# Optimization experiments

Hardware: AMD Instinct MI355X
Metric: run time of the kernel (lower is better)

The kernel has to match this reference:

```python
import jax, jax.numpy as jnp
from jax import lax
import numpy as np

IMG = 1024                      # image_size (square)
RPN_TRAIN_THRES = 0.5
RATIOS = jnp.array([0.5, 1.0, 2.0], jnp.float32)
SCALES = jnp.array([0.2, 0.4, 0.7], jnp.float32)
K_GT = 16


def _conv(x, w, b, stride):
    # NHWC x HWIO -> NHWC, VALID padding (keras Conv2D default)
    return lax.conv_general_dilated(x, w, (stride, stride), 'VALID',
                                    dimension_numbers=('NHWC', 'HWIO', 'NHWC')) + b


def _anchor_set():
    # [-w/2, -h/2, w/2, h/2] for 9 ratio/scale combos
    rs = jnp.sqrt(RATIOS)[:, None]                      # (3,1)
    ws = (SCALES[None, :] * rs).reshape(-1)             # (9,)
    hs = (SCALES[None, :] / rs).reshape(-1)
    return jnp.stack([ws, hs, ws, hs], axis=1) * 0.5 * jnp.array([-1.0, -1.0, 1.0, 1.0], jnp.float32)


def _anchors_pre(h, w):
    # mirrors generate_anchors_pre (incl. tf.transpose reversing axes -> (W,H,4));
    # feature map is square here so the layout matches the original.
    x = jnp.arange(0.0, 1.0, 1.0 / w, dtype=jnp.float32)
    y = jnp.arange(0.0, 1.0, 1.0 / h, dtype=jnp.float32)
    xx, yy = jnp.meshgrid(x, y)                         # (H,W)
    centers = jnp.stack([xx, yy, xx, yy], 0).transpose(2, 1, 0)  # (W,H,4)
    return centers[:, :, None, :] + _anchor_set()       # (W,H,9,4)


def _iou(b1, b2, gw, gh):
    gwh = jnp.array([gw, gh], jnp.float32)
    s1 = jnp.prod(b1[..., 2:] - b1[..., :2] + gwh, axis=-1)
    s2 = jnp.prod(b2[..., 2:] - b2[..., :2] + gwh, axis=-1)
    xa = jnp.maximum(b1[..., 0], b2[..., 0])
    ya = jnp.maximum(b1[..., 1], b2[..., 1])
    xb = jnp.minimum(b1[..., 2], b2[..., 2])
    yb = jnp.minimum(b1[..., 3], b2[..., 3])
    inter = jnp.maximum(xb - xa + gw, 0.0) * jnp.maximum(yb - ya + gh, 0.0)
    return inter / (s1 + s2 - inter)


def setup_inputs() -> dict:
    key = jax.random.key(0)
    ks = jax.random.split(key, 10)
    image = jax.random.uniform(ks[0], (1, IMG, IMG, 3), jnp.float32)
    cxy = jax.random.uniform(ks[1], (K_GT, 2), jnp.float32, 0.2, 0.8)
    wh = jax.random.uniform(ks[2], (K_GT, 2), jnp.float32, 0.1, 0.4)
    gt_boxes = jnp.concatenate([cxy - wh / 2, cxy + wh / 2], axis=1)  # (K,4) x1,y1,x2,y2
    Wb = jax.random.normal(ks[3], (4, 4, 3, 128), jnp.float32) * 0.05
    bb = jnp.zeros((128,), jnp.float32)
    Wi = jax.random.normal(ks[4], (3, 3, 128, 256), jnp.float32) * 0.05
    bi = jnp.zeros((256,), jnp.float32)
    Wc = jax.random.normal(ks[5], (1, 1, 256, 9), jnp.float32) * 0.05
    bc = jnp.zeros((9,), jnp.float32)
    Wr = jax.random.normal(ks[6], (1, 1, 256, 36), jnp.float32) * 0.05
    br = jnp.zeros((36,), jnp.float32)
    return {'image': image, 'gt_boxes': gt_boxes, 'Wb': Wb, 'bb': bb,
            'Wi': Wi, 'bi': bi, 'Wc': Wc, 'bc': bc, 'Wr': Wr, 'br': br}


def reference(image, gt_boxes, Wb, bb, Wi, bi, Wc, bc, Wr, br):
    feats = _conv(image, Wb, bb, 4)            # backbone: (1,256,256,128)
    fmap = _conv(feats, Wi, bi, 1)             # inter_conv: (1,254,254,256)
    fh, fw = fmap.shape[1], fmap.shape[2]
    gw = 1.0 / IMG
    gh = 1.0 / IMG
    anchors = _anchors_pre(fh, fw).reshape(-1, 4)          # (N,4), N = fh*fw*9
    inside = ((anchors[:, 0] >= 0.0) & (anchors[:, 1] >= 0.0) &
              (anchors[:, 2] < 1.0) & (anchors[:, 3] < 1.0))
    iou = _iou(anchors[:, None, :], gt_boxes[None, :, :], gw, gh)  # (N,K)
    max_iou = jnp.max(iou, axis=1)
    iou_in = jnp.where(inside[:, None], iou, -1.0)
    gt_max_iou = jnp.max(iou_in, axis=0)                   # (K,)
    is_gt_best = jnp.any((iou_in == gt_max_iou[None, :]) & inside[:, None], axis=1)
    pos = inside & (is_gt_best | (max_iou >= RPN_TRAIN_THRES))
    labels = jnp.where(inside, 0.0, -1.0)
    labels = jnp.where(pos, 1.0, labels)                   # (N,) in {-1,0,1}
    # RPN classification loss (BCE with logits) over labels != -1
    cls = _conv(fmap, Wc, bc, 1).reshape(-1)               # (N,)
    sel = (labels != -1.0).astype(jnp.float32)
    lbl = jnp.maximum(labels, 0.0)
    bce = lbl * jax.nn.softplus(-cls) + (1.0 - lbl) * jax.nn.softplus(cls)
    cls_loss = jnp.sum(bce * sel) / jnp.sum(sel)
    # smooth-L1 box loss, faithful to the original (it masks bbox_pred, not the diff)
    reg = _conv(fmap, Wr, br, 1).reshape(-1, 4)            # (N,4)
    m = pos.astype(jnp.float32)[:, None]                   # (N,1) bbox_mask
    ab = jnp.abs(reg * m)
    ss = (ab < 1.0).astype(jnp.float32)
    box_loss = ab * ab * 0.5 * ss + (ab - 0.5) * (1.0 - ss)
    bbox_loss = jnp.sum(box_loss) / jnp.sum(m)
    return cls_loss + bbox_loss
```

## Files before the change

kernel.cpp:

```cpp
#include <hip/hip_runtime.h>

#define F2      254
#define NPIX    (F2 * F2)
#define NANCH   (NPIX * 9)
#define KGT     16
#define GWC     (1.0f / 1024.0f)

typedef __attribute__((ext_vector_type(8))) short bf16x8;
typedef __attribute__((ext_vector_type(4))) float f32x4;

struct LossMap {
    int w0[9], h0[9], hsp[9], blk0[10];
};

__device__ unsigned short g_feats[256 * 256 * 128];
__device__ unsigned short g_cls[NPIX * 9];
__device__ unsigned short g_reg[NPIX * 36];
__device__ unsigned short g_W2s[36 * 3 * 64 * 8];
__device__ unsigned short g_Wbs[2 * 8 * 64 * 8];
__device__ float          g_b2[48];
__device__ float          g_acc[4];
__device__ unsigned       g_keys[KGT];
__device__ unsigned       g_done;

__device__ __forceinline__ float b2f(unsigned short h) {
    return __uint_as_float(((unsigned)h) << 16);
}
__device__ __forceinline__ unsigned short f2b(float f) {
    unsigned u = __float_as_uint(f);
    unsigned r = (u + 0x7FFFu + ((u >> 16) & 1u)) >> 16;
    return (unsigned short)r;
}

__device__ __forceinline__ void iou16(float x1, float y1, float x2, float y2,
                                      const float* __restrict__ gt, float* __restrict__ v) {
    float s1 = (x2 - x1 + GWC) * (y2 - y1 + GWC);
#pragma unroll
    for (int k = 0; k < KGT; ++k) {
        float gx1 = gt[k * 4 + 0], gy1 = gt[k * 4 + 1];
        float gx2 = gt[k * 4 + 2], gy2 = gt[k * 4 + 3];
        float s2 = (gx2 - gx1 + GWC) * (gy2 - gy1 + GWC);
        float xa = fmaxf(x1, gx1), ya = fmaxf(y1, gy1);
        float xb = fminf(x2, gx2), yb = fminf(y2, gy2);
        float iw = fmaxf(xb - xa + GWC, 0.0f);
        float ih = fmaxf(yb - ya + GWC, 0.0f);
        float inter = iw * ih;
        v[k] = inter / (s1 + s2 - inter);
    }
}

__device__ __forceinline__ void type_extent(int a, float* hw, float* hh) {
    int ri = a / 3, si = a - ri * 3;
    float rat = (ri == 0) ? 0.5f : (ri == 1) ? 1.0f : 2.0f;
    float scl = (si == 0) ? 0.2f : (si == 1) ? 0.4f : 0.7f;
    float rs = sqrtf(rat);
    *hw = scl * rs * 0.5f;
    *hh = scl / rs * 0.5f;
}

__global__ __launch_bounds__(256) void k_w2(const float* __restrict__ Wi,
                                            const float* __restrict__ bi,
                                            const float* __restrict__ Wc,
                                            const float* __restrict__ bc,
                                            const float* __restrict__ Wr,
                                            const float* __restrict__ br,
                                            const float* __restrict__ Wb,
                                            unsigned* out) {
    int t = threadIdx.x;
    int b = blockIdx.x;
    if (b >= 288) {
        int e = (b - 288) * 256 + t;
        int kt = e >> 9, nt = (e >> 6) & 7, l = e & 63;
        unsigned short w8[8];
#pragma unroll
        for (int j = 0; j < 8; ++j) {
            int k = kt * 32 + ((l >> 4) * 8) + j;
            int oc = nt * 16 + (l & 15);
            w8[j] = (k < 48) ? f2b(Wb[(size_t)k * 128 + oc]) : (unsigned short)0;
        }
        *(ulonglong2*)(g_Wbs + (size_t)e * 8) = *(ulonglong2*)w8;
        return;
    }
    __shared__ float wcr[256][48];
    if (b == 0) {
        if (t < 4) g_acc[t] = 0.0f;
        if (t >= 4 && t < 4 + KGT) g_keys[t - 4] = 0x407FFFFFu;
        if (t == 32) out[0] = 0x3F803F80u;
        if (t == 33) g_done = 0u;
    }
    for (int i = t; i < 2304; i += 256) wcr[i / 9][i % 9] = Wc[i];
    for (int i = t; i < 9216; i += 256) wcr[i / 36][9 + i % 36] = Wr[i];
    for (int i = t; i < 768; i += 256) wcr[i / 3][45 + i % 3] = 0.0f;
    __syncthreads();

    int wave = __builtin_amdgcn_readfirstlane(t >> 6);
    int lane = t & 63;
    int k = b * 4 + wave;
    int o = min(lane, 47);
    const float* wik = Wi + (size_t)k * 256;
    float acc = 0.0f;
#pragma unroll 8
    for (int oc = 0; oc < 256; ++oc)
        acc = fmaf(wik[oc], wcr[oc][o], acc);

    if (lane < 48) {
        int kt = k >> 5, r5 = k & 31, j = r5 & 7, lhi = r5 >> 3;
        int nt = o >> 4, llo = o & 15, l = lhi * 16 + llo;
        g_W2s[(size_t)((kt * 3 + nt) * 64 + l) * 8 + j] = f2b(acc);
    }
    if (b == 0 && t < 48) {
        float a2 = (t < 9) ? bc[t] : ((t < 45) ? br[t - 9] : 0.0f);
        for (int oc = 0; oc < 256; ++oc) a2 = fmaf(bi[oc], wcr[oc][t], a2);
        g_b2[t] = a2;
    }
}

__device__ __forceinline__ bf16x8 ld_a8(const float* ib, int kbase) {
    int r0 = kbase / 12, q0 = kbase - r0 * 12;
    unsigned short a8[8];
    float4 f0 = *(const float4*)(ib + (size_t)r0 * 3072 + q0);
    int k4 = kbase + 4;
    int r1 = k4 / 12, q1 = k4 - r1 * 12;
    float4 f1 = *(const float4*)(ib + (size_t)r1 * 3072 + q1);
    a8[0] = f2b(f0.x); a8[1] = f2b(f0.y); a8[2] = f2b(f0.z); a8[3] = f2b(f0.w);
    a8[4] = f2b(f1.x); a8[5] = f2b(f1.y); a8[6] = f2b(f1.z); a8[7] = f2b(f1.w);
    return *(bf16x8*)a8;
}

__global__ __launch_bounds__(256) void k_conv1gt(const float* __restrict__ img,
                                                 const float* __restrict__ bb,
                                                 const float* __restrict__ gt) {
    __shared__ float red[4][KGT];
    int t = threadIdx.x;
    if (blockIdx.x < 1024) {
        int l = t & 63;
        int quad = l >> 4;
        int tile = blockIdx.x * 4 + (t >> 6);
        int m0 = tile * 16;
        int p = m0 + (l & 15);
        int oy = p >> 8, ox = p & 255;
        const float* ib = img + ((size_t)oy * 4 * 1024 + (size_t)ox * 4) * 3;

        bf16x8 a0 = ld_a8(ib, quad * 8);
        bf16x8 a1 = (quad < 2) ? ld_a8(ib, 32 + quad * 8) : (bf16x8){0, 0, 0, 0, 0, 0, 0, 0};

        f32x4 acc[8];
#pragma unroll
        for (int nt = 0; nt < 8; ++nt) acc[nt] = (f32x4){0.0f, 0.0f, 0.0f, 0.0f};
#pragma unroll
        for (int nt = 0; nt < 8; ++nt) {
            bf16x8 b0 = *(const bf16x8*)(g_Wbs + (size_t)(nt * 64 + l) * 8);
            bf16x8 b1 = *(const bf16x8*)(g_Wbs + (size_t)((8 + nt) * 64 + l) * 8);
            acc[nt] = __builtin_amdgcn_mfma_f32_16x16x32_bf16(a0, b0, acc[nt], 0, 0, 0);
            acc[nt] = __builtin_amdgcn_mfma_f32_16x16x32_bf16(a1, b1, acc[nt], 0, 0, 0);
        }

        int n0 = l & 15;
        int mB = m0 + quad * 4;
#pragma unroll
        for (int nt = 0; nt < 8; ++nt) {
            int oc = nt * 16 + n0;
            float bias = bb[oc];
#pragma unroll
            for (int r = 0; r < 4; ++r) {
                g_feats[(size_t)(mB + r) * 128 + oc] = f2b(acc[nt][r] + bias);
            }
        }
    } else {
        int bid = blockIdx.x - 1024;
        int a = bid >> 5;
        int blk = bid & 31;
        float hw, hh;
        type_extent(a, &hw, &hh);
        float m16[KGT];
#pragma unroll
        for (int k = 0; k < KGT; ++k) m16[k] = -1.0f;
        for (int pix = blk * 256 + t; pix < NPIX; pix += 32 * 256) {
            int w = pix / F2, h = pix - w * F2;
            float cx = (float)w * (1.0f / 254.0f);
            float cy = (float)h * (1.0f / 254.0f);
            float x1 = cx - hw, y1 = cy - hh, x2 = cx + hw, y2 = cy + hh;
            bool inside = (x1 >= 0.0f) && (y1 >= 0.0f) && (x2 < 1.0f) && (y2 < 1.0f);
            if (__ballot(inside) == 0ull) continue;
            if (inside) {
                float v[KGT];
                iou16(x1, y1, x2, y2, gt, v);
#pragma unroll
                for (int k = 0; k < KGT; ++k) m16[k] = fmaxf(m16[k], v[k]);
            }
        }
#pragma unroll
        for (int k = 0; k < KGT; ++k) {
#pragma unroll
            for (int m = 32; m; m >>= 1) m16[k] = fmaxf(m16[k], __shfl_xor(m16[k], m, 64));
        }
        int lane = t & 63, wv = t >> 6;
        if (lane == 0) {
#pragma unroll
            for (int k = 0; k < KGT; ++k) red[wv][k] = m16[k];
        }
        __syncthreads();
        if (t < KGT) {
            float mx = fmaxf(fmaxf(red[0][t], red[1][t]), fmaxf(red[2][t], red[3][t]));
            unsigned u = __float_as_uint(mx);
            unsigned key = (u & 0x80000000u) ? ~u : (u | 0x80000000u);
            atomicMax(&g_keys[t], key);
        }
    }
}

__global__ __launch_bounds__(256) void k_convC() {
    __shared__ unsigned short Bs[12 * 1536];
    int t = threadIdx.x;
    int l = t & 63;
    int quad = l >> 4;
    int tile = blockIdx.x * 4 + (t >> 6);
    int m0 = tile * 32;
    int mA0 = min(m0 + (l & 15), NPIX - 1);
    int mA1 = min(m0 + 16 + (l & 15), NPIX - 1);
    int py0 = mA0 / F2, px0 = mA0 - py0 * F2;
    int py1 = mA1 / F2, px1 = mA1 - py1 * F2;

    f32x4 acc[2][3];
#pragma unroll
    for (int h = 0; h < 2; ++h)
#pragma unroll
        for (int nt = 0; nt < 3; ++nt) acc[h][nt] = (f32x4){0.0f, 0.0f, 0.0f, 0.0f};

    for (int c = 0; c < 3; ++c) {
        __syncthreads();
        {
            const uint4* src = (const uint4*)(g_W2s + (size_t)c * 18432);
            uint4* dst = (uint4*)Bs;
#pragma unroll
            for (int j = 0; j < 9; ++j) dst[t + 256 * j] = src[t + 256 * j];
        }
        __syncthreads();
#pragma unroll
        for (int i = 0; i < 12; ++i) {
            int kt = c * 12 + i;
            int pos = kt >> 2, kc = kt & 3;
            int ky = pos / 3, kx = pos - ky * 3;
            const unsigned short* ap0 =
                g_feats + ((size_t)(py0 + ky) * 256 + (px0 + kx)) * 128 + quad * 8 + kc * 32;
            const unsigned short* ap1 =
                g_feats + ((size_t)(py1 + ky) * 256 + (px1 + kx)) * 128 + quad * 8 + kc * 32;
            bf16x8 a0 = *(const bf16x8*)ap0;
            bf16x8 a1 = *(const bf16x8*)ap1;
            const unsigned short* bp = Bs + (size_t)i * 1536 + l * 8;
            bf16x8 b0 = *(const bf16x8*)(bp);
            bf16x8 b1 = *(const bf16x8*)(bp + 512);
            bf16x8 b2v = *(const bf16x8*)(bp + 1024);
            acc[0][0] = __builtin_amdgcn_mfma_f32_16x16x32_bf16(a0, b0, acc[0][0], 0, 0, 0);
            acc[0][1] = __builtin_amdgcn_mfma_f32_16x16x32_bf16(a0, b1, acc[0][1], 0, 0, 0);
            acc[0][2] = __builtin_amdgcn_mfma_f32_16x16x32_bf16(a0, b2v, acc[0][2], 0, 0, 0);
            acc[1][0] = __builtin_amdgcn_mfma_f32_16x16x32_bf16(a1, b0, acc[1][0], 0, 0, 0);
            acc[1][1] = __builtin_amdgcn_mfma_f32_16x16x32_bf16(a1, b1, acc[1][1], 0, 0, 0);
            acc[1][2] = __builtin_amdgcn_mfma_f32_16x16x32_bf16(a1, b2v, acc[1][2], 0, 0, 0);
        }
    }

    int n0 = l & 15;
#pragma unroll
    for (int h = 0; h < 2; ++h) {
        int mB = m0 + h * 16 + quad * 4;
#pragma unroll
        for (int nt = 0; nt < 3; ++nt) {
            int n = nt * 16 + n0;
            if (n >= 45) continue;
            float bias = g_b2[n];
#pragma unroll
            for (int r = 0; r < 4; ++r) {
                int m = mB + r;
                if (m < NPIX) {
                    float vv = acc[h][nt][r] + bias;
                    if (n < 9) g_cls[(size_t)m * 9 + n] = f2b(vv);
                    else       g_reg[(size_t)m * 36 + (n - 9)] = f2b(vv);
                }
            }
        }
    }
}

__global__ __launch_bounds__(256) void k_loss(const float* __restrict__ gt, unsigned* out,
                                              LossMap lm, int nblocks) {
    __shared__ float red[4][4];
    int t = threadIdx.x;
    int a = 0;
    while (a < 8 && (int)blockIdx.x >= lm.blk0[a + 1]) ++a;
    int idx = ((int)blockIdx.x - lm.blk0[a]) * 256 + t;
    int hsp = lm.hsp[a];
    int w = lm.w0[a] + idx / hsp;
    int h = lm.h0[a] + idx % hsp;
    float sb = 0.0f, ss = 0.0f, sx = 0.0f, sp = 0.0f;
    float hw, hh;
    type_extent(a, &hw, &hh);
    bool inside = false;
    float x1, y1, x2, y2;
    if (w < F2 && h < F2) {
        float cx = (float)w * (1.0f / 254.0f);
        float cy = (float)h * (1.0f / 254.0f);
        x1 = cx - hw; y1 = cy - hh; x2 = cx + hw; y2 = cy + hh;
        inside = (x1 >= 0.0f) && (y1 >= 0.0f) && (x2 < 1.0f) && (y2 < 1.0f);
    }
    if (__ballot(inside) != 0ull) {
        if (inside) {
            int pix = w * F2 + h;
            int n = pix * 9 + a;
            float v[KGT];
            iou16(x1, y1, x2, y2, gt, v);
            float maxi = -1.0f;
            bool best = false;
#pragma unroll
            for (int k = 0; k < KGT; ++k) {
                maxi = fmaxf(maxi, v[k]);
                unsigned e = g_keys[k];
                float gm = __uint_as_float((e & 0x80000000u) ? (e & 0x7FFFFFFFu) : ~e);
                best = best || (v[k] == gm);
            }
            bool ispos = best || (maxi >= 0.5f);
            float c = b2f(g_cls[n]);
            float z = ispos ? -c : c;
            sb = fmaxf(z, 0.0f) + log1pf(expf(-fabsf(z)));
            ss = 1.0f;
            if (ispos) {
                ushort4 rh = *(const ushort4*)(g_reg + (size_t)n * 4);
                float aa;
                aa = fabsf(b2f(rh.x)); sx += (aa < 1.0f) ? 0.5f * aa * aa : aa - 0.5f;
                aa = fabsf(b2f(rh.y)); sx += (aa < 1.0f) ? 0.5f * aa * aa : aa - 0.5f;
                aa = fabsf(b2f(rh.z)); sx += (aa < 1.0f) ? 0.5f * aa * aa : aa - 0.5f;
                aa = fabsf(b2f(rh.w)); sx += (aa < 1.0f) ? 0.5f * aa * aa : aa - 0.5f;
                sp = 1.0f;
            }
        }
    }
#pragma unroll
    for (int m = 32; m; m >>= 1) {
        sb += __shfl_xor(sb, m, 64);
        ss += __shfl_xor(ss, m, 64);
        sx += __shfl_xor(sx, m, 64);
        sp += __shfl_xor(sp, m, 64);
    }
    int lane = t & 63, wv = t >> 6;
    if (lane == 0) { red[wv][0] = sb; red[wv][1] = ss; red[wv][2] = sx; red[wv][3] = sp; }
    __syncthreads();
    if (t < 4) {
        float s = red[0][t] + red[1][t] + red[2][t] + red[3][t];
        atomicAdd(&g_acc[t], s);
    }
    __syncthreads();
    if (t == 0) {
        unsigned prev = atomicAdd(&g_done, 1u);
        if (prev == (unsigned)(nblocks - 1)) {
            float a0 = atomicAdd(&g_acc[0], 0.0f);
            float a1 = atomicAdd(&g_acc[1], 0.0f);
            float a2 = atomicAdd(&g_acc[2], 0.0f);
            float a3 = atomicAdd(&g_acc[3], 0.0f);
            float res = a0 / a1 + a2 / a3;
            unsigned lo = (unsigned)f2b(res);
            unsigned hi = __float_as_uint(res) >> 16;
            out[0] = (hi << 16) | lo;
        }
    }
}

extern "C" void kernel_launch(void* const* d_in, const int* in_sizes, int n_in,
                              void* d_out, int out_size, void* d_ws, size_t ws_size,
                              hipStream_t stream) {
    (void)in_sizes; (void)n_in; (void)out_size; (void)d_ws; (void)ws_size;
    const float* image = (const float*)d_in[0];
    const float* gt    = (const float*)d_in[1];
    const float* Wb    = (const float*)d_in[2];
    const float* bb    = (const float*)d_in[3];
    const float* Wi    = (const float*)d_in[4];
    const float* bi    = (const float*)d_in[5];
    const float* Wc    = (const float*)d_in[6];
    const float* bc    = (const float*)d_in[7];
    const float* Wr    = (const float*)d_in[8];
    const float* br    = (const float*)d_in[9];

    LossMap lm;
    int nb = 0;
    const float RAT[3] = {0.5f, 1.0f, 2.0f};
    const float SCL[3] = {0.2f, 0.4f, 0.7f};
    for (int a = 0; a < 9; ++a) {
        int ri = a / 3, si = a - ri * 3;
        float rs = sqrtf(RAT[ri]);
        float hw = SCL[si] * rs * 0.5f;
        float hh = SCL[si] / rs * 0.5f;
        int wa0 = (int)floorf(254.0f * hw) - 1; if (wa0 < 0) wa0 = 0;
        int wa1 = (int)ceilf(254.0f * (1.0f - hw)) + 1; if (wa1 > 253) wa1 = 253;
        int ha0 = (int)floorf(254.0f * hh) - 1; if (ha0 < 0) ha0 = 0;
        int ha1 = (int)ceilf(254.0f * (1.0f - hh)) + 1; if (ha1 > 253) ha1 = 253;
        int wspan = wa1 - wa0 + 1, hspan = ha1 - ha0 + 1;
        lm.w0[a] = wa0; lm.h0[a] = ha0; lm.hsp[a] = hspan;
        lm.blk0[a] = nb;
        nb += (wspan * hspan + 255) / 256;
    }
    lm.blk0[9] = nb;

    k_w2     <<<292, 256, 0, stream>>>(Wi, bi, Wc, bc, Wr, br, Wb, (unsigned*)d_out);
    k_conv1gt<<<1312, 256, 0, stream>>>(image, bb, gt);
    k_convC  <<<505, 256, 0, stream>>>();
    k_loss   <<<nb, 256, 0, stream>>>(gt, (unsigned*)d_out, lm, nb);
}
```

Baseline: 153.6 us.

## Fuse RPN head conv with loss and move GT-max pass into prep kernel

Fuses the classification/regression conv kernel with the loss kernel. Head outputs are staged in shared memory instead of being written to global g_cls/g_reg and read back. The per-GT max-IoU pass moves from the conv1 kernel into the weight-prep kernel, and conv1 block indices are remapped across XCDs. State reset now happens at the end of the last block rather than in a prep kernel, which cuts one launch and removes a global round trip. The cost is that the loss loop now scans all anchors per tile instead of only the bounded inside region, and it relies on static initialisers for the first call.

```diff
diff --git a/kernel.cpp b/kernel.cpp
--- a/kernel.cpp
+++ b/kernel.cpp
@@ -2,26 +2,23 @@
 
 #define F2      254
 #define NPIX    (F2 * F2)
-#define NANCH   (NPIX * 9)
 #define KGT     16
 #define GWC     (1.0f / 1024.0f)
 
 typedef __attribute__((ext_vector_type(8))) short bf16x8;
 typedef __attribute__((ext_vector_type(4))) float f32x4;
 
-struct LossMap {
-    int w0[9], h0[9], hsp[9], blk0[10];
-};
-
 __device__ unsigned short g_feats[256 * 256 * 128];
-__device__ unsigned short g_cls[NPIX * 9];
-__device__ unsigned short g_reg[NPIX * 36];
 __device__ unsigned short g_W2s[36 * 3 * 64 * 8];
 __device__ unsigned short g_Wbs[2 * 8 * 64 * 8];
 __device__ float          g_b2[48];
-__device__ float          g_acc[4];
-__device__ unsigned       g_keys[KGT];
-__device__ unsigned       g_done;
+__device__ float          g_acc[4] = {0.0f, 0.0f, 0.0f, 0.0f};
+__device__ unsigned       g_keys[KGT] = {
+    0x407FFFFFu, 0x407FFFFFu, 0x407FFFFFu, 0x407FFFFFu,
+    0x407FFFFFu, 0x407FFFFFu, 0x407FFFFFu, 0x407FFFFFu,
+    0x407FFFFFu, 0x407FFFFFu, 0x407FFFFFu, 0x407FFFFFu,
+    0x407FFFFFu, 0x407FFFFFu, 0x407FFFFFu, 0x407FFFFFu};
+__device__ unsigned       g_done = 0u;
 
 __device__ __forceinline__ float b2f(unsigned short h) {
     return __uint_as_float(((unsigned)h) << 16);
@@ -58,116 +55,21 @@
     *hh = scl / rs * 0.5f;
 }
 
-__global__ __launch_bounds__(256) void k_w2(const float* __restrict__ Wi,
-                                            const float* __restrict__ bi,
-                                            const float* __restrict__ Wc,
-                                            const float* __restrict__ bc,
-                                            const float* __restrict__ Wr,
-                                            const float* __restrict__ br,
-                                            const float* __restrict__ Wb,
-                                            unsigned* out) {
+__global__ __launch_bounds__(256) void k_prep(const float* __restrict__ Wi,
+                                              const float* __restrict__ bi,
+                                              const float* __restrict__ Wc,
+                                              const float* __restrict__ bc,
+                                              const float* __restrict__ Wr,
+                                              const float* __restrict__ br,
+                                              const float* __restrict__ Wb,
+                                              const float* __restrict__ gt) {
+    __shared__ float wcr[256][48];
+    __shared__ float red[4][KGT];
     int t = threadIdx.x;
     int b = blockIdx.x;
-    if (b >= 288) {
-        int e = (b - 288) * 256 + t;
-        int kt = e >> 9, nt = (e >> 6) & 7, l = e & 63;
-        unsigned short w8[8];
-#pragma unroll
-        for (int j = 0; j < 8; ++j) {
-            int k = kt * 32 + ((l >> 4) * 8) + j;
-            int oc = nt * 16 + (l & 15);
-            w8[j] = (k < 48) ? f2b(Wb[(size_t)k * 128 + oc]) : (unsigned short)0;
-        }
-        *(ulonglong2*)(g_Wbs + (size_t)e * 8) = *(ulonglong2*)w8;
-        return;
-    }
-    __shared__ float wcr[256][48];
-    if (b == 0) {
-        if (t < 4) g_acc[t] = 0.0f;
-        if (t >= 4 && t < 4 + KGT) g_keys[t - 4] = 0x407FFFFFu;
-        if (t == 32) out[0] = 0x3F803F80u;
-        if (t == 33) g_done = 0u;
-    }
-    for (int i = t; i < 2304; i += 256) wcr[i / 9][i % 9] = Wc[i];
-    for (int i = t; i < 9216; i += 256) wcr[i / 36][9 + i % 36] = Wr[i];
-    for (int i = t; i < 768; i += 256) wcr[i / 3][45 + i % 3] = 0.0f;
-    __syncthreads();
-
-    int wave = __builtin_amdgcn_readfirstlane(t >> 6);
-    int lane = t & 63;
-    int k = b * 4 + wave;
-    int o = min(lane, 47);
-    const float* wik = Wi + (size_t)k * 256;
-    float acc = 0.0f;
-#pragma unroll 8
-    for (int oc = 0; oc < 256; ++oc)
-        acc = fmaf(wik[oc], wcr[oc][o], acc);
-
-    if (lane < 48) {
-        int kt = k >> 5, r5 = k & 31, j = r5 & 7, lhi = r5 >> 3;
-        int nt = o >> 4, llo = o & 15, l = lhi * 16 + llo;
-        g_W2s[(size_t)((kt * 3 + nt) * 64 + l) * 8 + j] = f2b(acc);
-    }
-    if (b == 0 && t < 48) {
-        float a2 = (t < 9) ? bc[t] : ((t < 45) ? br[t - 9] : 0.0f);
-        for (int oc = 0; oc < 256; ++oc) a2 = fmaf(bi[oc], wcr[oc][t], a2);
-        g_b2[t] = a2;
-    }
-}
-
-__device__ __forceinline__ bf16x8 ld_a8(const float* ib, int kbase) {
-    int r0 = kbase / 12, q0 = kbase - r0 * 12;
-    unsigned short a8[8];
-    float4 f0 = *(const float4*)(ib + (size_t)r0 * 3072 + q0);
-    int k4 = kbase + 4;
-    int r1 = k4 / 12, q1 = k4 - r1 * 12;
-    float4 f1 = *(const float4*)(ib + (size_t)r1 * 3072 + q1);
-    a8[0] = f2b(f0.x); a8[1] = f2b(f0.y); a8[2] = f2b(f0.z); a8[3] = f2b(f0.w);
-    a8[4] = f2b(f1.x); a8[5] = f2b(f1.y); a8[6] = f2b(f1.z); a8[7] = f2b(f1.w);
-    return *(bf16x8*)a8;
-}
-
-__global__ __launch_bounds__(256) void k_conv1gt(const float* __restrict__ img,
-                                                 const float* __restrict__ bb,
-                                                 const float* __restrict__ gt) {
-    __shared__ float red[4][KGT];
-    int t = threadIdx.x;
-    if (blockIdx.x < 1024) {
-        int l = t & 63;
-        int quad = l >> 4;
-        int tile = blockIdx.x * 4 + (t >> 6);
-        int m0 = tile * 16;
-        int p = m0 + (l & 15);
-        int oy = p >> 8, ox = p & 255;
-        const float* ib = img + ((size_t)oy * 4 * 1024 + (size_t)ox * 4) * 3;
-
-        bf16x8 a0 = ld_a8(ib, quad * 8);
-        bf16x8 a1 = (quad < 2) ? ld_a8(ib, 32 + quad * 8) : (bf16x8){0, 0, 0, 0, 0, 0, 0, 0};
-
-        f32x4 acc[8];
-#pragma unroll
-        for (int nt = 0; nt < 8; ++nt) acc[nt] = (f32x4){0.0f, 0.0f, 0.0f, 0.0f};
-#pragma unroll
-        for (int nt = 0; nt < 8; ++nt) {
-            bf16x8 b0 = *(const bf16x8*)(g_Wbs + (size_t)(nt * 64 + l) * 8);
-            bf16x8 b1 = *(const bf16x8*)(g_Wbs + (size_t)((8 + nt) * 64 + l) * 8);
-            acc[nt] = __builtin_amdgcn_mfma_f32_16x16x32_bf16(a0, b0, acc[nt], 0, 0, 0);
-            acc[nt] = __builtin_amdgcn_mfma_f32_16x16x32_bf16(a1, b1, acc[nt], 0, 0, 0);
-        }
-
-        int n0 = l & 15;
-        int mB = m0 + quad * 4;
-#pragma unroll
-        for (int nt = 0; nt < 8; ++nt) {
-            int oc = nt * 16 + n0;
-            float bias = bb[oc];
-#pragma unroll
-            for (int r = 0; r < 4; ++r) {
-                g_feats[(size_t)(mB + r) * 128 + oc] = f2b(acc[nt][r] + bias);
-            }
-        }
-    } else {
-        int bid = blockIdx.x - 1024;
+
+    if (b >= 292) {
+        int bid = b - 292;
         int a = bid >> 5;
         int blk = bid & 31;
         float hw, hh;
@@ -206,15 +108,114 @@
             unsigned key = (u & 0x80000000u) ? ~u : (u | 0x80000000u);
             atomicMax(&g_keys[t], key);
         }
-    }
-}
-
-__global__ __launch_bounds__(256) void k_convC() {
-    __shared__ unsigned short Bs[12 * 1536];
+        return;
+    }
+
+    if (b >= 288) {
+        int e = (b - 288) * 256 + t;
+        int kt = e >> 9, nt = (e >> 6) & 7, l = e & 63;
+        unsigned short w8[8];
+#pragma unroll
+        for (int j = 0; j < 8; ++j) {
+            int k = kt * 32 + ((l >> 4) * 8) + j;
+            int oc = nt * 16 + (l & 15);
+            w8[j] = (k < 48) ? f2b(Wb[(size_t)k * 128 + oc]) : (unsigned short)0;
+        }
+        *(ulonglong2*)(g_Wbs + (size_t)e * 8) = *(ulonglong2*)w8;
+        return;
+    }
+
+    for (int i = t; i < 2304; i += 256) wcr[i / 9][i % 9] = Wc[i];
+    for (int i = t; i < 9216; i += 256) wcr[i / 36][9 + i % 36] = Wr[i];
+    for (int i = t; i < 768; i += 256) wcr[i / 3][45 + i % 3] = 0.0f;
+    __syncthreads();
+
+    int wave = __builtin_amdgcn_readfirstlane(t >> 6);
+    int lane = t & 63;
+    int k = b * 4 + wave;
+    int o = min(lane, 47);
+    const float* wik = Wi + (size_t)k * 256;
+    float acc = 0.0f;
+#pragma unroll 8
+    for (int oc = 0; oc < 256; ++oc)
+        acc = fmaf(wik[oc], wcr[oc][o], acc);
+
+    if (lane < 48) {
+        int kt = k >> 5, r5 = k & 31, j = r5 & 7, lhi = r5 >> 3;
+        int nt = o >> 4, llo = o & 15, l = lhi * 16 + llo;
+        g_W2s[(size_t)((kt * 3 + nt) * 64 + l) * 8 + j] = f2b(acc);
+    }
+    if (b == 0 && t < 48) {
+        float a2 = (t < 9) ? bc[t] : ((t < 45) ? br[t - 9] : 0.0f);
+        for (int oc = 0; oc < 256; ++oc) a2 = fmaf(bi[oc], wcr[oc][t], a2);
+        g_b2[t] = a2;
+    }
+}
+
+__device__ __forceinline__ bf16x8 ld_a8(const float* ib, int kbase) {
+    int r0 = kbase / 12, q0 = kbase - r0 * 12;
+    unsigned short a8[8];
+    float4 f0 = *(const float4*)(ib + (size_t)r0 * 3072 + q0);
+    int k4 = kbase + 4;
+    int r1 = k4 / 12, q1 = k4 - r1 * 12;
+    float4 f1 = *(const float4*)(ib + (size_t)r1 * 3072 + q1);
+    a8[0] = f2b(f0.x); a8[1] = f2b(f0.y); a8[2] = f2b(f0.z); a8[3] = f2b(f0.w);
+    a8[4] = f2b(f1.x); a8[5] = f2b(f1.y); a8[6] = f2b(f1.z); a8[7] = f2b(f1.w);
+    return *(bf16x8*)a8;
+}
+
+__global__ __launch_bounds__(256) void k_conv1(const float* __restrict__ img,
+                                               const float* __restrict__ bb) {
     int t = threadIdx.x;
+    int b = blockIdx.x;
+    int cid = ((b & 7) << 7) + (b >> 3);
     int l = t & 63;
     int quad = l >> 4;
-    int tile = blockIdx.x * 4 + (t >> 6);
+    int tile = cid * 4 + (t >> 6);
+    int m0 = tile * 16;
+    int p = m0 + (l & 15);
+    int oy = p >> 8, ox = p & 255;
+    const float* ib = img + ((size_t)oy * 4 * 1024 + (size_t)ox * 4) * 3;
+
+    bf16x8 a0 = ld_a8(ib, quad * 8);
+    bf16x8 a1 = (quad < 2) ? ld_a8(ib, 32 + quad * 8) : (bf16x8){0, 0, 0, 0, 0, 0, 0, 0};
+
+    f32x4 acc[8];
+#pragma unroll
+    for (int nt = 0; nt < 8; ++nt) acc[nt] = (f32x4){0.0f, 0.0f, 0.0f, 0.0f};
+#pragma unroll
+    for (int nt = 0; nt < 8; ++nt) {
+        bf16x8 b0 = *(const bf16x8*)(g_Wbs + (size_t)(nt * 64 + l) * 8);
+        bf16x8 b1 = *(const bf16x8*)(g_Wbs + (size_t)((8 + nt) * 64 + l) * 8);
+        acc[nt] = __builtin_amdgcn_mfma_f32_16x16x32_bf16(a0, b0, acc[nt], 0, 0, 0);
+        acc[nt] = __builtin_amdgcn_mfma_f32_16x16x32_bf16(a1, b1, acc[nt], 0, 0, 0);
+    }
+
+    int n0 = l & 15;
+    int mB = m0 + quad * 4;
+#pragma unroll
+    for (int nt = 0; nt < 8; ++nt) {
+        int oc = nt * 16 + n0;
+        float bias = bb[oc];
+#pragma unroll
+        for (int r = 0; r < 4; ++r) {
+            g_feats[(size_t)(mB + r) * 128 + oc] = f2b(acc[nt][r] + bias);
+        }
+    }
+}
+
+__global__ __launch_bounds__(256) void k_convC_loss(const float* __restrict__ gt,
+                                                    unsigned* __restrict__ out) {
+    __shared__ alignas(16) unsigned short Bs[12 * 1536];
+    __shared__ float redl[4][4];
+    int t = threadIdx.x;
+    int b = blockIdx.x;
+    int xcd = b & 7;
+    int cid = (xcd == 0) ? (b >> 3) : (64 + (xcd - 1) * 63 + (b >> 3));
+    int l = t & 63;
+    int quad = l >> 4;
+    int wv = t >> 6;
+    int tile = cid * 4 + wv;
     int m0 = tile * 32;
     int mA0 = min(m0 + (l & 15), NPIX - 1);
     int mA1 = min(m0 + 16 + (l & 15), NPIX - 1);
@@ -260,53 +261,41 @@
         }
     }
 
+    __syncthreads();
+    float (*S)[129] = (float (*)[129])(void*)Bs;
     int n0 = l & 15;
 #pragma unroll
     for (int h = 0; h < 2; ++h) {
-        int mB = m0 + h * 16 + quad * 4;
+        int plB = wv * 32 + h * 16 + quad * 4;
 #pragma unroll
         for (int nt = 0; nt < 3; ++nt) {
             int n = nt * 16 + n0;
-            if (n >= 45) continue;
             float bias = g_b2[n];
 #pragma unroll
-            for (int r = 0; r < 4; ++r) {
-                int m = mB + r;
-                if (m < NPIX) {
-                    float vv = acc[h][nt][r] + bias;
-                    if (n < 9) g_cls[(size_t)m * 9 + n] = f2b(vv);
-                    else       g_reg[(size_t)m * 36 + (n - 9)] = f2b(vv);
-                }
-            }
-        }
-    }
-}
-
-__global__ __launch_bounds__(256) void k_loss(const float* __restrict__ gt, unsigned* out,
-                                              LossMap lm, int nblocks) {
-    __shared__ float red[4][4];
-    int t = threadIdx.x;
-    int a = 0;
-    while (a < 8 && (int)blockIdx.x >= lm.blk0[a + 1]) ++a;
-    int idx = ((int)blockIdx.x - lm.blk0[a]) * 256 + t;
-    int hsp = lm.hsp[a];
-    int w = lm.w0[a] + idx / hsp;
-    int h = lm.h0[a] + idx % hsp;
+            for (int r = 0; r < 4; ++r) S[n][plB + r] = acc[h][nt][r] + bias;
+        }
+    }
+    __syncthreads();
+
+    int m0b = cid * 128;
     float sb = 0.0f, ss = 0.0f, sx = 0.0f, sp = 0.0f;
-    float hw, hh;
-    type_extent(a, &hw, &hh);
-    bool inside = false;
-    float x1, y1, x2, y2;
-    if (w < F2 && h < F2) {
-        float cx = (float)w * (1.0f / 254.0f);
-        float cy = (float)h * (1.0f / 254.0f);
-        x1 = cx - hw; y1 = cy - hh; x2 = cx + hw; y2 = cy + hh;
-        inside = (x1 >= 0.0f) && (y1 >= 0.0f) && (x2 < 1.0f) && (y2 < 1.0f);
-    }
-    if (__ballot(inside) != 0ull) {
+    for (int idx = t; idx < 1152; idx += 256) {
+        int a = idx >> 7;
+        int pl = idx & 127;
+        int m = m0b + pl;
+        float hw, hhf;
+        type_extent(a, &hw, &hhf);
+        bool inside = false;
+        float x1 = 0.0f, y1 = 0.0f, x2 = 0.0f, y2 = 0.0f;
+        if (m < NPIX) {
+            int pw = m / F2, ph = m - pw * F2;
+            float cx = (float)pw * (1.0f / 254.0f);
+            float cy = (float)ph * (1.0f / 254.0f);
+            x1 = cx - hw; y1 = cy - hhf; x2 = cx + hw; y2 = cy + hhf;
+            inside = (x1 >= 0.0f) && (y1 >= 0.0f) && (x2 < 1.0f) && (y2 < 1.0f);
+        }
+        if (__ballot(inside) == 0ull) continue;
         if (inside) {
-            int pix = w * F2 + h;
-            int n = pix * 9 + a;
             float v[KGT];
             iou16(x1, y1, x2, y2, gt, v);
             float maxi = -1.0f;
@@ -319,39 +308,39 @@
                 best = best || (v[k] == gm);
             }
             bool ispos = best || (maxi >= 0.5f);
-            float c = b2f(g_cls[n]);
+            float c = b2f(f2b(S[a][pl]));
             float z = ispos ? -c : c;
-            sb = fmaxf(z, 0.0f) + log1pf(expf(-fabsf(z)));
-            ss = 1.0f;
+            sb += fmaxf(z, 0.0f) + log1pf(expf(-fabsf(z)));
+            ss += 1.0f;
             if (ispos) {
-                ushort4 rh = *(const ushort4*)(g_reg + (size_t)n * 4);
                 float aa;
-                aa = fabsf(b2f(rh.x)); sx += (aa < 1.0f) ? 0.5f * aa * aa : aa - 0.5f;
-                aa = fabsf(b2f(rh.y)); sx += (aa < 1.0f) ? 0.5f * aa * aa : aa - 0.5f;
-                aa = fabsf(b2f(rh.z)); sx += (aa < 1.0f) ? 0.5f * aa * aa : aa - 0.5f;
-                aa = fabsf(b2f(rh.w)); sx += (aa < 1.0f) ? 0.5f * aa * aa : aa - 0.5f;
-                sp = 1.0f;
+                aa = fabsf(b2f(f2b(S[9 + 4 * a + 0][pl]))); sx += (aa < 1.0f) ? 0.5f * aa * aa : aa - 0.5f;
+                aa = fabsf(b2f(f2b(S[9 + 4 * a + 1][pl]))); sx += (aa < 1.0f) ? 0.5f * aa * aa : aa - 0.5f;
+                aa = fabsf(b2f(f2b(S[9 + 4 * a + 2][pl]))); sx += (aa < 1.0f) ? 0.5f * aa * aa : aa - 0.5f;
+                aa = fabsf(b2f(f2b(S[9 + 4 * a + 3][pl]))); sx += (aa < 1.0f) ? 0.5f * aa * aa : aa - 0.5f;
+                sp += 1.0f;
             }
         }
     }
-#pragma unroll
-    for (int m = 32; m; m >>= 1) {
-        sb += __shfl_xor(sb, m, 64);
-        ss += __shfl_xor(ss, m, 64);
-        sx += __shfl_xor(sx, m, 64);
-        sp += __shfl_xor(sp, m, 64);
-    }
-    int lane = t & 63, wv = t >> 6;
-    if (lane == 0) { red[wv][0] = sb; red[wv][1] = ss; red[wv][2] = sx; red[wv][3] = sp; }
+
+#pragma unroll
+    for (int mm = 32; mm; mm >>= 1) {
+        sb += __shfl_xor(sb, mm, 64);
+        ss += __shfl_xor(ss, mm, 64);
+        sx += __shfl_xor(sx, mm, 64);
+        sp += __shfl_xor(sp, mm, 64);
+    }
+    int lane = t & 63;
+    if (lane == 0) { redl[wv][0] = sb; redl[wv][1] = ss; redl[wv][2] = sx; redl[wv][3] = sp; }
     __syncthreads();
     if (t < 4) {
-        float s = red[0][t] + red[1][t] + red[2][t] + red[3][t];
+        float s = redl[0][t] + redl[1][t] + redl[2][t] + redl[3][t];
         atomicAdd(&g_acc[t], s);
     }
     __syncthreads();
     if (t == 0) {
         unsigned prev = atomicAdd(&g_done, 1u);
-        if (prev == (unsigned)(nblocks - 1)) {
+        if (prev == 504u) {
             float a0 = atomicAdd(&g_acc[0], 0.0f);
             float a1 = atomicAdd(&g_acc[1], 0.0f);
             float a2 = atomicAdd(&g_acc[2], 0.0f);
@@ -360,6 +349,10 @@
             unsigned lo = (unsigned)f2b(res);
             unsigned hi = __float_as_uint(res) >> 16;
             out[0] = (hi << 16) | lo;
+            g_acc[0] = 0.0f; g_acc[1] = 0.0f; g_acc[2] = 0.0f; g_acc[3] = 0.0f;
+#pragma unroll
+            for (int k = 0; k < KGT; ++k) g_keys[k] = 0x407FFFFFu;
+            g_done = 0u;
         }
     }
 }
@@ -379,28 +372,7 @@
     const float* Wr    = (const float*)d_in[8];
     const float* br    = (const float*)d_in[9];
 
-    LossMap lm;
-    int nb = 0;
-    const float RAT[3] = {0.5f, 1.0f, 2.0f};
-    const float SCL[3] = {0.2f, 0.4f, 0.7f};
-    for (int a = 0; a < 9; ++a) {
-        int ri = a / 3, si = a - ri * 3;
-        float rs = sqrtf(RAT[ri]);
-        float hw = SCL[si] * rs * 0.5f;
-        float hh = SCL[si] / rs * 0.5f;
-        int wa0 = (int)floorf(254.0f * hw) - 1; if (wa0 < 0) wa0 = 0;
-        int wa1 = (int)ceilf(254.0f * (1.0f - hw)) + 1; if (wa1 > 253) wa1 = 253;
-        int ha0 = (int)floorf(254.0f * hh) - 1; if (ha0 < 0) ha0 = 0;
-        int ha1 = (int)ceilf(254.0f * (1.0f - hh)) + 1; if (ha1 > 253) ha1 = 253;
-        int wspan = wa1 - wa0 + 1, hspan = ha1 - ha0 + 1;
-        lm.w0[a] = wa0; lm.h0[a] = ha0; lm.hsp[a] = hspan;
-        lm.blk0[a] = nb;
-        nb += (wspan * hspan + 255) / 256;
-    }
-    lm.blk0[9] = nb;
-
-    k_w2     <<<292, 256, 0, stream>>>(Wi, bi, Wc, bc, Wr, br, Wb, (unsigned*)d_out);
-    k_conv1gt<<<1312, 256, 0, stream>>>(image, bb, gt);
-    k_convC  <<<505, 256, 0, stream>>>();
-    k_loss   <<<nb, 256, 0, stream>>>(gt, (unsigned*)d_out, lm, nb);
-}
+    k_prep      <<<580, 256, 0, stream>>>(Wi, bi, Wc, bc, Wr, br, Wb, gt);
+    k_conv1     <<<1024, 256, 0, stream>>>(image, bb);
+    k_convC_loss<<<505, 256, 0, stream>>>(gt, (unsigned*)d_out);
+}
```

After: 132.4 us. 1.16x faster.
